# Kernel optimization log

Hardware: AMD Instinct MI355X
Metric: run time of the kernel (lower is better)

Reference implementation:

```python
import jax, jax.numpy as jnp
import numpy as np

NJ, NS = 30000, 12000            # num job / skill nodes
E_JS, E_SJ, E_SS = 300000, 300000, 150000
SBERT, HID, OUT = 384, 128, 128
H = 2                             # GAT heads (concat=True)
NEG_SLOPE = 0.2


def setup_inputs() -> dict:
    key = jax.random.key(0)
    ks = iter(jax.random.split(key, 64))
    nrm = lambda shape, s=1.0: jax.random.normal(next(ks), shape, jnp.float32) * s
    ridx = lambda n, hi: jax.random.randint(next(ks), (n,), 0, hi, jnp.int32)
    W = 0.05  # weight scale to keep activations sane across layers
    return dict(
        x_job=nrm((NJ, SBERT)), x_skill=nrm((NS, SBERT)),
        ei_js_src=ridx(E_JS, NJ), ei_js_dst=ridx(E_JS, NS),
        ei_sj_src=ridx(E_SJ, NS), ei_sj_dst=ridx(E_SJ, NJ),
        ei_ss_src=ridx(E_SS, NS), ei_ss_dst=ridx(E_SS, NS),
        query=nrm((SBERT,)),
        W0_job=nrm((SBERT, HID), W), b0_job=jnp.zeros((HID,), jnp.float32),
        g0_job=jnp.ones((HID,), jnp.float32), be0_job=jnp.zeros((HID,), jnp.float32),
        W0_skill=nrm((SBERT, HID), W), b0_skill=jnp.zeros((HID,), jnp.float32),
        g0_skill=jnp.ones((HID,), jnp.float32), be0_skill=jnp.zeros((HID,), jnp.float32),
        gat_Ws=nrm((2, 3, HID, H * HID), W), gat_Wd=nrm((2, 3, HID, H * HID), W),
        gat_as=nrm((2, 3, H, HID), W), gat_ad=nrm((2, 3, H, HID), W),
        gat_b=jnp.zeros((2, 3, H * HID), jnp.float32),
        inter_W=nrm((2, 2, H * HID, HID), W), inter_b=jnp.zeros((2, 2, HID), jnp.float32),
        Wjf=nrm((HID, OUT), W), bjf=jnp.zeros((OUT,), jnp.float32),
        Wq=nrm((SBERT, OUT), W), bq=jnp.zeros((OUT,), jnp.float32),
    )


def _layer_norm(x, g, b):
    mu = x.mean(-1, keepdims=True)
    var = ((x - mu) ** 2).mean(-1, keepdims=True)
    return (x - mu) * jax.lax.rsqrt(var + 1e-5) * g + b


def _gat(x_src, x_dst, src, dst, Ws, Wd, a_s, a_d, bias, num_dst):
    # PyG GATConv: lin_src/lin_dst (no bias), additive attention, scatter-softmax over dst.
    hs = (x_src @ Ws).reshape(-1, H, HID)            # [Ns,H,C]
    hd = (x_dst @ Wd).reshape(-1, H, HID)            # [Nd,H,C]
    e = jax.nn.leaky_relu((hs * a_s).sum(-1)[src] + (hd * a_d).sum(-1)[dst], NEG_SLOPE)  # [E,H]
    m = jax.ops.segment_max(e, dst, num_segments=num_dst)
    p = jnp.exp(e - m[dst])
    den = jax.ops.segment_sum(p, dst, num_segments=num_dst)
    w = p / (den[dst] + 1e-16)                       # [E,H]
    out = jax.ops.segment_sum(hs[src] * w[:, :, None], dst, num_segments=num_dst)
    return out.reshape(num_dst, H * HID) + bias


def _forward(x_job, x_skill, query,
             W0_job, b0_job, g0_job, be0_job, W0_skill, b0_skill, g0_skill, be0_skill,
             gat_Ws, gat_Wd, gat_as, gat_ad, gat_b, inter_W, inter_b, Wjf, bjf, Wq, bq,
             ei_js_src, ei_js_dst, ei_sj_src, ei_sj_dst, ei_ss_src, ei_ss_dst):
    # initial per-type lin + LN + relu (dropout = identity in eval)
    xj = jax.nn.relu(_layer_norm(x_job @ W0_job + b0_job, g0_job, be0_job))
    xs = jax.nn.relu(_layer_norm(x_skill @ W0_skill + b0_skill, g0_skill, be0_skill))
    # skill->skill relation adds self loops (src == dst node type)
    loops = jnp.arange(NS, dtype=jnp.int32)
    ss_src = jnp.concatenate([ei_ss_src, loops])
    ss_dst = jnp.concatenate([ei_ss_dst, loops])
    for i in range(2):  # num_layers
        o_s = (_gat(xj, xs, ei_js_src, ei_js_dst, gat_Ws[i, 0], gat_Wd[i, 0],
                    gat_as[i, 0], gat_ad[i, 0], gat_b[i, 0], NS)
               + _gat(xs, xs, ss_src, ss_dst, gat_Ws[i, 2], gat_Wd[i, 2],
                      gat_as[i, 2], gat_ad[i, 2], gat_b[i, 2], NS))  # HeteroConv aggr='sum'
        o_j = _gat(xs, xj, ei_sj_src, ei_sj_dst, gat_Ws[i, 1], gat_Wd[i, 1],
                   gat_as[i, 1], gat_ad[i, 1], gat_b[i, 1], NJ)
        xj = jax.nn.relu(o_j @ inter_W[i, 0] + inter_b[i, 0])
        xs = jax.nn.relu(o_s @ inter_W[i, 1] + inter_b[i, 1])
    job_emb = xj @ Wjf + bjf                          # [NJ,OUT]
    q = query @ Wq + bq                               # [OUT]
    scores = job_emb @ q                              # [NJ]
    return scores, job_emb, q


def reference(x_job, x_skill, ei_js_src, ei_js_dst, ei_sj_src, ei_sj_dst,
              ei_ss_src, ei_ss_dst, query,
              W0_job, b0_job, g0_job, be0_job, W0_skill, b0_skill, g0_skill, be0_skill,
              gat_Ws, gat_Wd, gat_as, gat_ad, gat_b, inter_W, inter_b,
              Wjf, bjf, Wq, bq):
    return _forward(x_job, x_skill, query,
                    W0_job, b0_job, g0_job, be0_job, W0_skill, b0_skill, g0_skill, be0_skill,
                    gat_Ws, gat_Wd, gat_as, gat_ad, gat_b, inter_W, inter_b, Wjf, bjf, Wq, bq,
                    ei_js_src, ei_js_dst, ei_sj_src, ei_sj_dst, ei_ss_src, ei_ss_dst)
```

## Files before the change

kernel.cpp:

```cpp
#include <hip/hip_runtime.h>
#include <hip/hip_bf16.h>
#include <math.h>

#define NJ 30000
#define NS 12000
#define E_JS 300000
#define E_SJ 300000
#define E_SS 150000
#define ETOT (E_JS + E_SJ + E_SS + NS)
#define NBINS (NS + NJ + NS)
#define NBUK ((NBINS + 63) / 64)
#define SBERT 384
#define HIST_NB 512
#define SCAT_NB 120
#define CAST_MATS 14
#define CAST_BPM 48
#define PREP_CAST (CAST_MATS * CAST_BPM)
#define PREP_WA   (PREP_CAST + 12)
#define PREP_QV   PREP_WA
#define PREP_GB   (PREP_QV + 1)
#define PREP_HIST (PREP_GB + 1)

static inline int cdiv(int a, int b) { return (a + b - 1) / b; }

typedef __attribute__((ext_vector_type(8))) short bf8_t;
typedef __attribute__((ext_vector_type(4))) float f4_t;
typedef unsigned short u16;

__device__ inline float bf2f(unsigned short u) {
    union { unsigned int i; float f; } z; z.i = ((unsigned int)u) << 16; return z.f;
}
__device__ inline unsigned short f2bf(float f) {
    unsigned int x = __float_as_uint(f);
    unsigned int r = (x + 0x7fffu + ((x >> 16) & 1u)) >> 16;
    return (unsigned short)r;
}

__device__ inline void edge_decode(int e, const int* js_src, const int* js_dst,
                                   const int* sj_src, const int* sj_dst,
                                   const int* ss_src, const int* ss_dst,
                                   int& src, int& bin) {
    if (e < E_JS) { src = js_src[e]; bin = js_dst[e]; }
    else if (e < E_JS + E_SJ) { int i = e - E_JS; src = sj_src[i]; bin = NS + sj_dst[i]; }
    else if (e < E_JS + E_SJ + E_SS) { int i = e - E_JS - E_SJ; src = ss_src[i]; bin = NS + NJ + ss_dst[i]; }
    else { int i = e - E_JS - E_SJ - E_SS; src = i; bin = NS + NJ + i; }
}

struct CastT { const float* src; unsigned short* dst; int K; int N; int srcLd; int dstLd; };
struct PrepArgs {
    CastT m[CAST_MATS];
    const float* Ws; const float* as_; const float* Wd; const float* ad_;
    float* wsa; float* wda; int* bcnt;
    const float* query; const float* Wq; const float* bq; float* qv;
    const float* gat_b; float* gbS;
    const int* js_src; const int* js_dst;
    const int* sj_src; const int* sj_dst;
    const int* ss_src; const int* ss_dst;
};

__global__ __launch_bounds__(256) void k_prep(PrepArgs A) {
    __shared__ float ldt[32][33];
    __shared__ int lh[NBUK];
    int b = blockIdx.x;
    if (b < PREP_CAST) {
        int mi = b / CAST_BPM, bx = b % CAST_BPM;
        CastT cm = A.m[mi];
        int tilesN = cm.N >> 5;
        int total = (cm.K >> 5) * tilesN;
        if (bx >= total) return;
        int tk = bx / tilesN, tn = bx % tilesN;
        int k0 = tk * 32, n0 = tn * 32;
        int col = threadIdx.x & 31;
        int row0 = threadIdx.x >> 5;
#pragma unroll
        for (int r = 0; r < 4; ++r) {
            int kk = row0 + r * 8;
            ldt[kk][col] = cm.src[(size_t)(k0 + kk) * cm.srcLd + n0 + col];
        }
        __syncthreads();
#pragma unroll
        for (int r = 0; r < 4; ++r) {
            int nn = row0 + r * 8;
            cm.dst[(size_t)(n0 + nn) * cm.dstLd + k0 + col] = f2bf(ldt[col][nn]);
        }
    } else if (b < PREP_WA) {
        int id = (b - PREP_CAST) * 256 + threadIdx.x;
        if (id >= 2 * 1536) return;
        int which = id / 1536;
        int r = id % 1536;
        int lr = r / 256;
        int kh = r % 256;
        int k = kh / 2, h = kh % 2;
        const float* W = which ? A.Wd : A.Ws;
        const float* a = which ? A.ad_ : A.as_;
        const float* wrow = W + ((size_t)(lr * 128 + k)) * 256 + h * 128;
        const float* arow = a + (size_t)(lr * 2 + h) * 128;
        float acc = 0.f;
        for (int c2 = 0; c2 < 128; ++c2) acc += wrow[c2] * arow[c2];
        (which ? A.wda : A.wsa)[lr * 256 + k * 2 + h] = acc;
    } else if (b == PREP_QV) {
        int c = threadIdx.x;
        if (c < 128) {
            float acc = A.bq[c];
            for (int k = 0; k < SBERT; ++k) acc += A.query[k] * A.Wq[(size_t)k * 128 + c];
            A.qv[c] = acc;
        }
    } else if (b == PREP_GB) {
        int c = threadIdx.x;
        if (c < 256) A.gbS[c] = A.gat_b[c] + A.gat_b[512 + c];
    } else {
        int t = threadIdx.x;
        for (int i = t; i < NBUK; i += 256) lh[i] = 0;
        __syncthreads();
        int hb = b - PREP_HIST;
        for (int e = hb * 256 + t; e < ETOT; e += HIST_NB * 256) {
            int src, bin;
            edge_decode(e, A.js_src, A.js_dst, A.sj_src, A.sj_dst, A.ss_src, A.ss_dst, src, bin);
            atomicAdd(&lh[bin >> 6], 1);
        }
        __syncthreads();
        for (int i = t; i < NBUK; i += 256) {
            int v = lh[i];
            if (v) atomicAdd(&A.bcnt[i], v);
        }
    }
}

struct GJob {
    const void* X; const unsigned short* Wt;
    const float* bias; const float* gamma; const float* beta;
    void* Y; int M; int K; int N; int ldY; int srcf32;
    const float* qv; float* sc;
    int aMode = 0;
    const float* wav0 = nullptr; const float* wav1 = nullptr;
    const float* wav2 = nullptr; const float* wav3 = nullptr;
    float* aOut = nullptr; int aStride = 0;
};
struct GPair { GJob a; GJob b; int blocksA; };

template <int EPI>
__device__ void mgemm_body(const GPair& P, int bx) {
    int mb = bx;
    GJob g = (mb < P.blocksA) ? P.a : P.b;
    if (mb >= P.blocksA) mb -= P.blocksA;
    const int row0 = mb * 64;

    __shared__ __align__(16) unsigned short Al[2][64][40];
    __shared__ __align__(16) unsigned short Bl[2][128][40];
    const int t = threadIdx.x;
    const int wave = t >> 6, lane = t & 63;
    const int q = lane >> 4, c = lane & 15;
    const int K = g.K;
    const int rA = t >> 2, cc8 = (t & 3) * 8;
    const int grA = row0 + rA;
    const bool inM = grA < g.M;
    const float* Xf = (const float*)g.X;

    f4_t acc[8];
#pragma unroll
    for (int nt = 0; nt < 8; ++nt) acc[nt] = (f4_t){0.f, 0.f, 0.f, 0.f};

    float4 a0[2], a1[2];
    uint4 b0[2], b1[2];

    auto LOAD = [&](int s, int k0) {
        if (inM) {
            const float* p = &Xf[(size_t)grA * K + k0 + cc8];
            a0[s] = *(const float4*)p;
            a1[s] = *(const float4*)(p + 4);
        } else {
            a0[s] = make_float4(0.f, 0.f, 0.f, 0.f);
            a1[s] = a0[s];
        }
        b0[s] = *(const uint4*)&g.Wt[(size_t)rA * K + k0 + cc8];
        b1[s] = *(const uint4*)&g.Wt[(size_t)(64 + rA) * K + k0 + cc8];
    };
    auto STORE = [&](int s, int cur) {
        ushort4 lo = make_ushort4(f2bf(a0[s].x), f2bf(a0[s].y), f2bf(a0[s].z), f2bf(a0[s].w));
        ushort4 hi = make_ushort4(f2bf(a1[s].x), f2bf(a1[s].y), f2bf(a1[s].z), f2bf(a1[s].w));
        *(ushort4*)&Al[cur][rA][cc8] = lo;
        *(ushort4*)&Al[cur][rA][cc8 + 4] = hi;
        *(uint4*)&Bl[cur][rA][cc8] = b0[s];
        *(uint4*)&Bl[cur][64 + rA][cc8] = b1[s];
    };
    auto MF = [&](int cur) {
        bf8_t af = *(const bf8_t*)&Al[cur][wave * 16 + c][q * 8];
#pragma unroll
        for (int nt = 0; nt < 8; ++nt) {
            bf8_t bfr = *(const bf8_t*)&Bl[cur][nt * 16 + c][q * 8];
            acc[nt] = __builtin_amdgcn_mfma_f32_16x16x32_bf16(af, bfr, acc[nt], 0, 0, 0);
        }
    };

    LOAD(0, 0);
    LOAD(1, 32);
    int cur = 0;
    for (int k0 = 0; k0 < K; k0 += 64) {
        STORE(0, cur);
        __syncthreads();
        if (k0 + 64 < K) LOAD(0, k0 + 64);
        MF(cur);
        cur ^= 1;
        STORE(1, cur);
        __syncthreads();
        if (k0 + 96 < K) LOAD(1, k0 + 96);
        MF(cur);
        cur ^= 1;
    }

    float bcol[8], gcol[8], becol[8];
#pragma unroll
    for (int nt = 0; nt < 8; ++nt) {
        bcol[nt] = g.bias[nt * 16 + c];
        if constexpr (EPI == 3) {
            gcol[nt] = g.gamma[nt * 16 + c];
            becol[nt] = g.beta[nt * 16 + c];
        }
    }

#pragma unroll
    for (int r = 0; r < 4; ++r) {
        int grow = row0 + wave * 16 + q * 4 + r;
        float v[8];
#pragma unroll
        for (int nt = 0; nt < 8; ++nt) v[nt] = acc[nt][r] + bcol[nt];
        if constexpr (EPI == 3) {
            float s = 0.f, ss = 0.f;
#pragma unroll
            for (int nt = 0; nt < 8; ++nt) { s += v[nt]; ss += v[nt] * v[nt]; }
#pragma unroll
            for (int m = 8; m >= 1; m >>= 1) {
                s += __shfl_xor(s, m, 64);
                ss += __shfl_xor(ss, m, 64);
            }
            float mu = s * (1.f / 128.f);
            float var = ss * (1.f / 128.f) - mu * mu;
            float rs = rsqrtf(var + 1e-5f);
#pragma unroll
            for (int nt = 0; nt < 8; ++nt)
                v[nt] = fmaxf((v[nt] - mu) * rs * gcol[nt] + becol[nt], 0.f);
        }
        if (g.aMode > 0) {
            float pa[8];
#pragma unroll
            for (int i = 0; i < 8; ++i) pa[i] = 0.f;
#pragma unroll
            for (int nt = 0; nt < 8; ++nt) {
                int col = nt * 16 + c;
                float2 w0 = *(const float2*)&g.wav0[col * 2];
                pa[0] += v[nt] * w0.x; pa[1] += v[nt] * w0.y;
                if (g.aMode > 1) {
                    float2 w1 = *(const float2*)&g.wav1[col * 2];
                    pa[2] += v[nt] * w1.x; pa[3] += v[nt] * w1.y;
                }
                if (g.aMode > 2) {
                    float2 w2 = *(const float2*)&g.wav2[col * 2];
                    float2 w3 = *(const float2*)&g.wav3[col * 2];
                    pa[4] += v[nt] * w2.x; pa[5] += v[nt] * w2.y;
                    pa[6] += v[nt] * w3.x; pa[7] += v[nt] * w3.y;
                }
            }
#pragma unroll
            for (int m = 8; m >= 1; m >>= 1) {
                pa[0] += __shfl_xor(pa[0], m, 64); pa[1] += __shfl_xor(pa[1], m, 64);
                pa[2] += __shfl_xor(pa[2], m, 64); pa[3] += __shfl_xor(pa[3], m, 64);
                pa[4] += __shfl_xor(pa[4], m, 64); pa[5] += __shfl_xor(pa[5], m, 64);
                pa[6] += __shfl_xor(pa[6], m, 64); pa[7] += __shfl_xor(pa[7], m, 64);
            }
            if (c == 0 && grow < g.M) {
                float* ao = &g.aOut[(size_t)grow * g.aStride];
                ao[0] = pa[0]; ao[1] = pa[1];
                if (g.aMode > 1) { ao[2] = pa[2]; ao[3] = pa[3]; }
                if (g.aMode > 2) { ao[4] = pa[4]; ao[5] = pa[5]; ao[6] = pa[6]; ao[7] = pa[7]; }
            }
        }
        if (grow < g.M) {
            unsigned short* Y = (unsigned short*)g.Y;
#pragma unroll
            for (int nt = 0; nt < 8; ++nt)
                Y[(size_t)grow * g.ldY + nt * 16 + c] = f2bf(v[nt]);
        }
    }
}

__global__ __launch_bounds__(256) void k_scan(
    const int* __restrict__ bcnt, int* __restrict__ bukoff, int* __restrict__ bukcur) {
    __shared__ int sd[256];
    int t = threadIdx.x;
    int i0 = t * 4;
    int v0 = (i0 < NBUK) ? bcnt[i0] : 0;
    int v1 = (i0 + 1 < NBUK) ? bcnt[i0 + 1] : 0;
    int v2 = (i0 + 2 < NBUK) ? bcnt[i0 + 2] : 0;
    int v3 = (i0 + 3 < NBUK) ? bcnt[i0 + 3] : 0;
    int csum = v0 + v1 + v2 + v3;
    sd[t] = csum;
    __syncthreads();
    for (int off = 1; off < 256; off <<= 1) {
        int tmp = (t >= off) ? sd[t - off] : 0;
        __syncthreads();
        sd[t] += tmp;
        __syncthreads();
    }
    int excl = sd[t] - csum;
    int p0 = excl, p1 = excl + v0, p2 = excl + v0 + v1, p3 = excl + v0 + v1 + v2;
    if (i0 < NBUK) { bukoff[i0] = p0; bukcur[i0] = p0; }
    if (i0 + 1 < NBUK) { bukoff[i0 + 1] = p1; bukcur[i0 + 1] = p1; }
    if (i0 + 2 < NBUK) { bukoff[i0 + 2] = p2; bukcur[i0 + 2] = p2; }
    if (i0 + 3 < NBUK) { bukoff[i0 + 3] = p3; bukcur[i0 + 3] = p3; }
    if (t == 0) bukoff[NBUK] = ETOT;
}

__global__ __launch_bounds__(256) void k_lin0_scat(
    GPair P, int gemmBlocks,
    const int* __restrict__ js_src, const int* __restrict__ js_dst,
    const int* __restrict__ sj_src, const int* __restrict__ sj_dst,
    const int* __restrict__ ss_src, const int* __restrict__ ss_dst,
    int* __restrict__ bukcur, uint2* __restrict__ pairs) {
    if (blockIdx.x < (unsigned)gemmBlocks) {
        mgemm_body<3>(P, blockIdx.x);
        return;
    }
    __shared__ int lh[NBUK];
    __shared__ int lbase[NBUK];
    int t = threadIdx.x;
    int sb = blockIdx.x - gemmBlocks;
    const int CH = (ETOT + SCAT_NB - 1) / SCAT_NB;
    const int beg = sb * CH;
    const int endi = (beg + CH < ETOT) ? beg + CH : ETOT;
    for (int i = t; i < NBUK; i += 256) lh[i] = 0;
    __syncthreads();
    for (int e = beg + t; e < endi; e += 256) {
        int src, bin;
        edge_decode(e, js_src, js_dst, sj_src, sj_dst, ss_src, ss_dst, src, bin);
        atomicAdd(&lh[bin >> 6], 1);
    }
    __syncthreads();
    for (int i = t; i < NBUK; i += 256) {
        int v = lh[i];
        lbase[i] = v ? atomicAdd(&bukcur[i], v) : 0;
    }
    __syncthreads();
    for (int i = t; i < NBUK; i += 256) lh[i] = 0;
    __syncthreads();
    for (int e = beg + t; e < endi; e += 256) {
        int src, bin;
        edge_decode(e, js_src, js_dst, sj_src, sj_dst, ss_src, ss_dst, src, bin);
        int bu = bin >> 6;
        int pos = lbase[bu] + atomicAdd(&lh[bu], 1);
        pairs[pos] = make_uint2((unsigned)src, (unsigned)bin);
    }
}

__global__ __launch_bounds__(256) void k_finalize(
    const uint2* __restrict__ pairs, const int* __restrict__ bukoff,
    int* __restrict__ offs, int* __restrict__ esrc) {
    int b = blockIdx.x, t = threadIdx.x;
    int base = bukoff[b], endi = bukoff[b + 1];
    __shared__ int cnt[64], excl[64], curs[64];
    if (t < 64) cnt[t] = 0;
    __syncthreads();
    for (int i = base + t; i < endi; i += 256)
        atomicAdd(&cnt[pairs[i].y & 63], 1);
    __syncthreads();
    if (t < 64) {
        int v = cnt[t];
        int inc = v;
#pragma unroll
        for (int off = 1; off < 64; off <<= 1) {
            int tmp = __shfl_up(inc, off, 64);
            if (t >= off) inc += tmp;
        }
        excl[t] = inc - v;
        curs[t] = inc - v;
    }
    __syncthreads();
    for (int i = base + t; i < endi; i += 256) {
        uint2 p = pairs[i];
        int lb = p.y & 63;
        int pos = atomicAdd(&curs[lb], 1);
        esrc[base + pos] = (int)p.x;
    }
    if (t < 64) {
        int bin = b * 64 + t;
        if (bin < NBINS) offs[bin] = base + excl[t];
    }
    if (b == 0 && t == 0) offs[NBINS] = ETOT;
}

__device__ inline void fm8(float p0, float p1, uint4 u, float a0[8], float a1[8]) {
    float x0 = __uint_as_float(u.x << 16);
    float x1 = __uint_as_float(u.x & 0xffff0000u);
    float x2 = __uint_as_float(u.y << 16);
    float x3 = __uint_as_float(u.y & 0xffff0000u);
    float x4 = __uint_as_float(u.z << 16);
    float x5 = __uint_as_float(u.z & 0xffff0000u);
    float x6 = __uint_as_float(u.w << 16);
    float x7 = __uint_as_float(u.w & 0xffff0000u);
    a0[0] += p0 * x0; a0[1] += p0 * x1; a0[2] += p0 * x2; a0[3] += p0 * x3;
    a0[4] += p0 * x4; a0[5] += p0 * x5; a0[6] += p0 * x6; a0[7] += p0 * x7;
    a1[0] += p1 * x0; a1[1] += p1 * x1; a1[2] += p1 * x2; a1[3] += p1 * x3;
    a1[4] += p1 * x4; a1[5] += p1 * x5; a1[6] += p1 * x6; a1[7] += p1 * x7;
}

__device__ inline void rel_run(
    const int* __restrict__ esrc, int beg, int end,
    const float* __restrict__ aSrc, int aShift, int aOff, float adx, float ady,
    const unsigned short* __restrict__ rows, int colOff, int g,
    float a0[8], float a1[8], float& den0, float& den1) {
    int j = beg;
    for (; j + 8 <= end; j += 8) {
        int s0 = esrc[j + g];
        int s1 = esrc[j + 4 + g];
        uint4 u0 = *(const uint4*)&rows[(unsigned)s0 * 128 + colOff];
        uint4 u1 = *(const uint4*)&rows[(unsigned)s1 * 128 + colOff];
        float2 f0 = *(const float2*)&aSrc[((unsigned)s0 << aShift) + aOff];
        float2 f1 = *(const float2*)&aSrc[((unsigned)s1 << aShift) + aOff];
        float e00 = f0.x + adx; e00 = e00 > 0.f ? e00 : 0.2f * e00;
        float e01 = f0.y + ady; e01 = e01 > 0.f ? e01 : 0.2f * e01;
        float e10 = f1.x + adx; e10 = e10 > 0.f ? e10 : 0.2f * e10;
        float e11 = f1.y + ady; e11 = e11 > 0.f ? e11 : 0.2f * e11;
        float p00 = __expf(e00), p01 = __expf(e01);
        float p10 = __expf(e10), p11 = __expf(e11);
        fm8(p00, p01, u0, a0, a1);
        fm8(p10, p11, u1, a0, a1);
        den0 += p00 + p10; den1 += p01 + p11;
    }
    for (; j < end; j += 4) {
        int e = j + g;
        bool ok = e < end;
        int s = esrc[ok ? e : j];
        uint4 u = *(const uint4*)&rows[(unsigned)s * 128 + colOff];
        float2 f = *(const float2*)&aSrc[((unsigned)s << aShift) + aOff];
        float e0 = f.x + adx; e0 = e0 > 0.f ? e0 : 0.2f * e0;
        float e1 = f.y + ady; e1 = e1 > 0.f ? e1 : 0.2f * e1;
        float p0 = ok ? __expf(e0) : 0.f;
        float p1 = ok ? __expf(e1) : 0.f;
        fm8(p0, p1, u, a0, a1);
        den0 += p0; den1 += p1;
    }
}

__device__ inline void store8(unsigned short* dst, const float v[8]) {
    uint4 o;
    o.x = (unsigned)f2bf(v[0]) | ((unsigned)f2bf(v[1]) << 16);
    o.y = (unsigned)f2bf(v[2]) | ((unsigned)f2bf(v[3]) << 16);
    o.z = (unsigned)f2bf(v[4]) | ((unsigned)f2bf(v[5]) << 16);
    o.w = (unsigned)f2bf(v[6]) | ((unsigned)f2bf(v[7]) << 16);
    *(uint4*)dst = o;
}

__device__ inline void finish_store(float a0[8], float a1[8], float den0, float den1,
                                    int lane, unsigned short* base) {
    float d0 = den0; d0 += __shfl_xor(d0, 16, 64); d0 += __shfl_xor(d0, 32, 64);
    float d1 = den1; d1 += __shfl_xor(d1, 16, 64); d1 += __shfl_xor(d1, 32, 64);
    float s0 = 1.f / (d0 + 1e-16f), s1 = 1.f / (d1 + 1e-16f);
    float o0[8], o1[8];
#pragma unroll
    for (int i = 0; i < 8; ++i) {
        float t0 = a0[i]; t0 += __shfl_xor(t0, 16, 64); t0 += __shfl_xor(t0, 32, 64);
        float t1 = a1[i]; t1 += __shfl_xor(t1, 16, 64); t1 += __shfl_xor(t1, 32, 64);
        o0[i] = t0 * s0; o1[i] = t1 * s1;
    }
    if ((lane >> 4) == 0) {
        store8(base, o0);
        store8(base + 128, o1);
    }
}

__global__ __launch_bounds__(256) void k_gather_all(
    const int* __restrict__ offs, const int* __restrict__ esrc,
    const float* __restrict__ aJ, const float* __restrict__ aS,
    const unsigned short* __restrict__ rowsJ,
    const unsigned short* __restrict__ rowsS,
    unsigned short* __restrict__ aggS,
    unsigned short* __restrict__ aggJ,
    int jobOnly) {
    int wave = threadIdx.x >> 6, lane = threadIdx.x & 63;
    int idx = blockIdx.x * 4 + wave;
    int g = lane >> 4, cl = lane & 15;
    int colOff = cl * 8;

    float a0[8], a1[8], den0, den1;

    if (jobOnly) {
        if (idx >= NJ) return;
        int d = idx;
#pragma unroll
        for (int i = 0; i < 8; ++i) { a0[i] = 0.f; a1[i] = 0.f; }
        den0 = den1 = 0.f;
        int bb = NS + d;
        float2 ad = *(const float2*)&aJ[(unsigned)d * 4 + 2];
        rel_run(esrc, offs[bb], offs[bb + 1], aS, 3, 4, ad.x, ad.y, rowsS, colOff, g, a0, a1, den0, den1);
        finish_store(a0, a1, den0, den1, lane, &aggJ[(size_t)d * 256 + colOff]);
        return;
    }
    if (idx < NS) {
        int d = idx;
#pragma unroll
        for (int i = 0; i < 8; ++i) { a0[i] = 0.f; a1[i] = 0.f; }
        den0 = den1 = 0.f;
        float2 adA = *(const float2*)&aS[(unsigned)d * 8 + 2];
        rel_run(esrc, offs[d], offs[d + 1], aJ, 2, 0, adA.x, adA.y, rowsJ, colOff, g, a0, a1, den0, den1);
        finish_store(a0, a1, den0, den1, lane, &aggS[(size_t)d * 512 + colOff]);
#pragma unroll
        for (int i = 0; i < 8; ++i) { a0[i] = 0.f; a1[i] = 0.f; }
        den0 = den1 = 0.f;
        int bb = NS + NJ + d;
        float2 adB = *(const float2*)&aS[(unsigned)d * 8 + 6];
        rel_run(esrc, offs[bb], offs[bb + 1], aS, 3, 0, adB.x, adB.y, rowsS, colOff, g, a0, a1, den0, den1);
        finish_store(a0, a1, den0, den1, lane, &aggS[(size_t)d * 512 + 256 + colOff]);
    } else if (idx < NS + NJ) {
        int d = idx - NS;
#pragma unroll
        for (int i = 0; i < 8; ++i) { a0[i] = 0.f; a1[i] = 0.f; }
        den0 = den1 = 0.f;
        int bb = NS + d;
        float2 ad = *(const float2*)&aJ[(unsigned)d * 4 + 2];
        rel_run(esrc, offs[bb], offs[bb + 1], aS, 3, 4, ad.x, ad.y, rowsS, colOff, g, a0, a1, den0, den1);
        finish_store(a0, a1, den0, den1, lane, &aggJ[(size_t)d * 256 + colOff]);
    }
}

struct FJob {
    const unsigned short* X; int K1; int M;
    const unsigned short* Wt1; const float* bias1;
    const unsigned short* Wt2; const float* bias2;
    const float* wa; float* aOut; int aStride;
    unsigned short* Y2;
};
struct FPair { FJob a; FJob b; int blocksA; };

__global__ __launch_bounds__(256) void k_fused2(FPair P) {
    int mb = blockIdx.x;
    FJob g = (mb < P.blocksA) ? P.a : P.b;
    if (mb >= P.blocksA) mb -= P.blocksA;
    const int row0 = mb * 64;
    const int K1 = g.K1;

    __shared__ __align__(16) unsigned short Al[64][40];
    __shared__ __align__(16) unsigned short Bl[128][40];
    __shared__ __align__(16) unsigned short Y1l[4][64][40];
    const int t = threadIdx.x;
    const int wave = t >> 6, lane = t & 63;
    const int q = lane >> 4, c = lane & 15;

    f4_t acc2[8];
#pragma unroll
    for (int nt = 0; nt < 8; ++nt) acc2[nt] = (f4_t){0.f, 0.f, 0.f, 0.f};

    for (int np = 0; np < 2; ++np) {
        f4_t acc[8];
#pragma unroll
        for (int nt = 0; nt < 8; ++nt) acc[nt] = (f4_t){0.f, 0.f, 0.f, 0.f};
        for (int k0 = 0; k0 < K1; k0 += 32) {
#pragma unroll
            for (int it = 0; it < 3; ++it) {
                int idx = t + it * 256;
                int r = idx >> 2, cc = (idx & 3) * 8;
                if (r < 64) {
                    int gr = row0 + r;
                    uint4 va = (gr < g.M) ? *(const uint4*)&g.X[(size_t)gr * K1 + k0 + cc]
                                          : make_uint4(0u, 0u, 0u, 0u);
                    *(uint4*)&Al[r][cc] = va;
                } else {
                    int br = r - 64;
                    *(uint4*)&Bl[br][cc] = *(const uint4*)&g.Wt1[(size_t)(np * 128 + br) * K1 + k0 + cc];
                }
            }
            __syncthreads();
            bf8_t af = *(const bf8_t*)&Al[wave * 16 + c][q * 8];
#pragma unroll
            for (int nt = 0; nt < 8; ++nt) {
                bf8_t bfr = *(const bf8_t*)&Bl[nt * 16 + c][q * 8];
                acc[nt] = __builtin_amdgcn_mfma_f32_16x16x32_bf16(af, bfr, acc[nt], 0, 0, 0);
            }
            __syncthreads();
        }
        float bcol[8];
#pragma unroll
        for (int nt = 0; nt < 8; ++nt) bcol[nt] = g.bias1[np * 128 + nt * 16 + c];
#pragma unroll
        for (int r = 0; r < 4; ++r) {
            int row = wave * 16 + q * 4 + r;
#pragma unroll
            for (int nt = 0; nt < 8; ++nt)
                Y1l[nt >> 1][row][(nt & 1) * 16 + c] = f2bf(acc[nt][r] + bcol[nt]);
        }
        __syncthreads();
        for (int k0 = 0; k0 < 128; k0 += 32) {
#pragma unroll
            for (int it = 0; it < 2; ++it) {
                int idx = t + it * 256;
                int br = idx >> 2, cc = (idx & 3) * 8;
                *(uint4*)&Bl[br][cc] = *(const uint4*)&g.Wt2[(size_t)br * 256 + np * 128 + k0 + cc];
            }
            __syncthreads();
            bf8_t af = *(const bf8_t*)&Y1l[k0 >> 5][wave * 16 + c][q * 8];
#pragma unroll
            for (int nt = 0; nt < 8; ++nt) {
                bf8_t bfr = *(const bf8_t*)&Bl[nt * 16 + c][q * 8];
                acc2[nt] = __builtin_amdgcn_mfma_f32_16x16x32_bf16(af, bfr, acc2[nt], 0, 0, 0);
            }
            __syncthreads();
        }
    }

    float b2[8];
#pragma unroll
    for (int nt = 0; nt < 8; ++nt) b2[nt] = g.bias2[nt * 16 + c];
#pragma unroll
    for (int r = 0; r < 4; ++r) {
        int grow = row0 + wave * 16 + q * 4 + r;
        float v[8];
#pragma unroll
        for (int nt = 0; nt < 8; ++nt) v[nt] = fmaxf(acc2[nt][r] + b2[nt], 0.f);
        if (g.wa) {
            float pa0 = 0.f, pa1 = 0.f;
#pragma unroll
            for (int nt = 0; nt < 8; ++nt) {
                float2 w0 = *(const float2*)&g.wa[(nt * 16 + c) * 2];
                pa0 += v[nt] * w0.x; pa1 += v[nt] * w0.y;
            }
#pragma unroll
            for (int m = 8; m >= 1; m >>= 1) {
                pa0 += __shfl_xor(pa0, m, 64);
                pa1 += __shfl_xor(pa1, m, 64);
            }
            if (c == 0 && grow < g.M) {
                g.aOut[(size_t)grow * g.aStride + 0] = pa0;
                g.aOut[(size_t)grow * g.aStride + 1] = pa1;
            }
        }
        if (g.Y2 && grow < g.M) {
#pragma unroll
            for (int nt = 0; nt < 8; ++nt)
                g.Y2[(size_t)grow * 128 + nt * 16 + c] = f2bf(v[nt]);
        }
    }
}

struct F3 {
    const unsigned short* X; int M;
    const unsigned short* Wt1; const float* bias1;
    const unsigned short* Wt2; const float* bias2;
    const unsigned short* Wt3; const float* bias3;
    const float* qv; float* sc; float* Y;
};

__global__ __launch_bounds__(256) void k_fused3(F3 g) {
    int mb = blockIdx.x;
    const int row0 = mb * 64;
    __shared__ __align__(16) unsigned short Al[64][40];
    __shared__ __align__(16) unsigned short Bl[128][40];
    __shared__ __align__(16) unsigned short Yl[4][64][40];
    const int t = threadIdx.x;
    const int wave = t >> 6, lane = t & 63;
    const int q = lane >> 4, c = lane & 15;

    f4_t acc2[8];
#pragma unroll
    for (int nt = 0; nt < 8; ++nt) acc2[nt] = (f4_t){0.f, 0.f, 0.f, 0.f};

    for (int np = 0; np < 2; ++np) {
        f4_t acc[8];
#pragma unroll
        for (int nt = 0; nt < 8; ++nt) acc[nt] = (f4_t){0.f, 0.f, 0.f, 0.f};
        for (int k0 = 0; k0 < 256; k0 += 32) {
#pragma unroll
            for (int it = 0; it < 3; ++it) {
                int idx = t + it * 256;
                int r = idx >> 2, cc = (idx & 3) * 8;
                if (r < 64) {
                    int gr = row0 + r;
                    uint4 va = (gr < g.M) ? *(const uint4*)&g.X[(size_t)gr * 256 + k0 + cc]
                                          : make_uint4(0u, 0u, 0u, 0u);
                    *(uint4*)&Al[r][cc] = va;
                } else {
                    int br = r - 64;
                    *(uint4*)&Bl[br][cc] = *(const uint4*)&g.Wt1[(size_t)(np * 128 + br) * 256 + k0 + cc];
                }
            }
            __syncthreads();
            bf8_t af = *(const bf8_t*)&Al[wave * 16 + c][q * 8];
#pragma unroll
            for (int nt = 0; nt < 8; ++nt) {
                bf8_t bfr = *(const bf8_t*)&Bl[nt * 16 + c][q * 8];
                acc[nt] = __builtin_amdgcn_mfma_f32_16x16x32_bf16(af, bfr, acc[nt], 0, 0, 0);
            }
            __syncthreads();
        }
        float bcol[8];
#pragma unroll
        for (int nt = 0; nt < 8; ++nt) bcol[nt] = g.bias1[np * 128 + nt * 16 + c];
#pragma unroll
        for (int r = 0; r < 4; ++r) {
            int row = wave * 16 + q * 4 + r;
#pragma unroll
            for (int nt = 0; nt < 8; ++nt)
                Yl[nt >> 1][row][(nt & 1) * 16 + c] = f2bf(acc[nt][r] + bcol[nt]);
        }
        __syncthreads();
        for (int k0 = 0; k0 < 128; k0 += 32) {
#pragma unroll
            for (int it = 0; it < 2; ++it) {
                int idx = t + it * 256;
                int br = idx >> 2, cc = (idx & 3) * 8;
                *(uint4*)&Bl[br][cc] = *(const uint4*)&g.Wt2[(size_t)br * 256 + np * 128 + k0 + cc];
            }
            __syncthreads();
            bf8_t af = *(const bf8_t*)&Yl[k0 >> 5][wave * 16 + c][q * 8];
#pragma unroll
            for (int nt = 0; nt < 8; ++nt) {
                bf8_t bfr = *(const bf8_t*)&Bl[nt * 16 + c][q * 8];
                acc2[nt] = __builtin_amdgcn_mfma_f32_16x16x32_bf16(af, bfr, acc2[nt], 0, 0, 0);
            }
            __syncthreads();
        }
    }

    {
        float b2[8];
#pragma unroll
        for (int nt = 0; nt < 8; ++nt) b2[nt] = g.bias2[nt * 16 + c];
#pragma unroll
        for (int r = 0; r < 4; ++r) {
            int row = wave * 16 + q * 4 + r;
#pragma unroll
            for (int nt = 0; nt < 8; ++nt)
                Yl[nt >> 1][row][(nt & 1) * 16 + c] = f2bf(fmaxf(acc2[nt][r] + b2[nt], 0.f));
        }
        __syncthreads();
    }

    f4_t acc3[8];
#pragma unroll
    for (int nt = 0; nt < 8; ++nt) acc3[nt] = (f4_t){0.f, 0.f, 0.f, 0.f};
    for (int k0 = 0; k0 < 128; k0 += 32) {
#pragma unroll
        for (int it = 0; it < 2; ++it) {
            int idx = t + it * 256;
            int br = idx >> 2, cc = (idx & 3) * 8;
            *(uint4*)&Bl[br][cc] = *(const uint4*)&g.Wt3[(size_t)br * 128 + k0 + cc];
        }
        __syncthreads();
        bf8_t af = *(const bf8_t*)&Yl[k0 >> 5][wave * 16 + c][q * 8];
#pragma unroll
        for (int nt = 0; nt < 8; ++nt) {
            bf8_t bfr = *(const bf8_t*)&Bl[nt * 16 + c][q * 8];
            acc3[nt] = __builtin_amdgcn_mfma_f32_16x16x32_bf16(af, bfr, acc3[nt], 0, 0, 0);
        }
        __syncthreads();
    }
    float b3[8], qcol[8];
#pragma unroll
    for (int nt = 0; nt < 8; ++nt) {
        b3[nt] = g.bias3[nt * 16 + c];
        qcol[nt] = g.qv[nt * 16 + c];
    }
#pragma unroll
    for (int r = 0; r < 4; ++r) {
        int grow = row0 + wave * 16 + q * 4 + r;
        float v[8];
#pragma unroll
        for (int nt = 0; nt < 8; ++nt) v[nt] = acc3[nt][r] + b3[nt];
        float part = 0.f;
#pragma unroll
        for (int nt = 0; nt < 8; ++nt) part += v[nt] * qcol[nt];
#pragma unroll
        for (int m = 8; m >= 1; m >>= 1) part += __shfl_xor(part, m, 64);
        if (grow < g.M) {
            if (c == 0) g.sc[grow] = part;
#pragma unroll
            for (int nt = 0; nt < 8; ++nt)
                g.Y[(size_t)grow * 128 + nt * 16 + c] = v[nt];
        }
    }
}

extern "C" void kernel_launch(void* const* d_in, const int* in_sizes, int n_in,
                              void* d_out, int out_size, void* d_ws, size_t ws_size,
                              hipStream_t stream) {
    const float* x_job   = (const float*)d_in[0];
    const float* x_skill = (const float*)d_in[1];
    const int* js_src = (const int*)d_in[2];
    const int* js_dst = (const int*)d_in[3];
    const int* sj_src = (const int*)d_in[4];
    const int* sj_dst = (const int*)d_in[5];
    const int* ss_src = (const int*)d_in[6];
    const int* ss_dst = (const int*)d_in[7];
    const float* query    = (const float*)d_in[8];
    const float* W0_job   = (const float*)d_in[9];
    const float* b0_job   = (const float*)d_in[10];
    const float* g0_job   = (const float*)d_in[11];
    const float* be0_job  = (const float*)d_in[12];
    const float* W0_skill = (const float*)d_in[13];
    const float* b0_skill = (const float*)d_in[14];
    const float* g0_skill = (const float*)d_in[15];
    const float* be0_skill= (const float*)d_in[16];
    const float* gat_Ws = (const float*)d_in[17];
    const float* gat_Wd = (const float*)d_in[18];
    const float* gat_as = (const float*)d_in[19];
    const float* gat_ad = (const float*)d_in[20];
    const float* gat_b  = (const float*)d_in[21];
    const float* inter_W = (const float*)d_in[22];
    const float* inter_b = (const float*)d_in[23];
    const float* Wjf = (const float*)d_in[24];
    const float* bjf = (const float*)d_in[25];
    const float* Wq  = (const float*)d_in[26];
    const float* bq  = (const float*)d_in[27];

    char* w = (char*)d_ws;
    auto alloc = [&](size_t bytes) -> void* {
        void* p = (void*)w;
        w += (bytes + 255) & ~(size_t)255;
        return p;
    };
    u16* xj   = (u16*)alloc((size_t)NJ * 128 * 2);
    u16* xs   = (u16*)alloc((size_t)NS * 128 * 2);
    u16* xs1  = (u16*)alloc((size_t)NS * 128 * 2);
    u16* aggJ  = (u16*)alloc((size_t)NJ * 256 * 2);
    u16* aggJ1 = (u16*)alloc((size_t)NJ * 256 * 2);
    u16* aggS  = (u16*)alloc((size_t)NS * 512 * 2);
    u16* WtW0j = (u16*)alloc((size_t)SBERT * 128 * 2);
    u16* WtW0s = (u16*)alloc((size_t)SBERT * 128 * 2);
    u16* WsS1  = (u16*)alloc((size_t)256 * 512 * 2);
    u16* WsJ0  = (u16*)alloc((size_t)256 * 256 * 2);
    u16* WsJ1  = (u16*)alloc((size_t)256 * 256 * 2);
    u16* WtI00 = (u16*)alloc((size_t)128 * 256 * 2);
    u16* WtI01 = (u16*)alloc((size_t)128 * 256 * 2);
    u16* WtI10 = (u16*)alloc((size_t)128 * 256 * 2);
    u16* WtJf  = (u16*)alloc((size_t)128 * 128 * 2);
    float* gbS = (float*)alloc(256 * 4);
    float* aJ = (float*)alloc((size_t)NJ * 4 * 4);
    float* aS = (float*)alloc((size_t)NS * 8 * 4);
    float* wsa = (float*)alloc(6 * 256 * 4);
    float* wda = (float*)alloc(6 * 256 * 4);
    int* bcnt   = (int*)alloc((size_t)NBUK * 4);
    int* bukoff = (int*)alloc((size_t)(NBUK + 1) * 4);
    int* bukcur = (int*)alloc((size_t)NBUK * 4);
    uint2* pairs = (uint2*)alloc((size_t)ETOT * 8);
    int* offs = (int*)alloc((size_t)(NBINS + 1) * 4);
    int* esrc = (int*)alloc((size_t)ETOT * 4);

    float* out = (float*)d_out;
    float* scores  = out;
    float* job_emb = out + NJ;
    float* qv      = out + NJ + (size_t)NJ * 128;

    const int mbJ = cdiv(NJ, 64);
    const int mbS = cdiv(NS, 64);
    const int gemmB = mbJ + mbS;

    hipMemsetAsync(bcnt, 0, (size_t)NBUK * 4, stream);
    hipMemsetAsync(WsS1, 0, (size_t)256 * 512 * 2, stream);
    hipMemsetAsync(WsJ0, 0, (size_t)256 * 256 * 2, stream);
    hipMemsetAsync(WsJ1, 0, (size_t)256 * 256 * 2, stream);

    {
        const size_t WS = (size_t)128 * 256;
        const size_t IW = (size_t)256 * 128;
        PrepArgs A;
        A.m[0]  = {W0_job,   WtW0j, SBERT, 128, 128, SBERT};
        A.m[1]  = {W0_skill, WtW0s, SBERT, 128, 128, SBERT};
        A.m[2]  = {gat_Ws + 0 * WS,       WsS1,                       128, 128, 256, 512};
        A.m[3]  = {gat_Ws + 0 * WS + 128, WsS1 + 128 * 512 + 128,     128, 128, 256, 512};
        A.m[4]  = {gat_Ws + 2 * WS,       WsS1 + 256,                 128, 128, 256, 512};
        A.m[5]  = {gat_Ws + 2 * WS + 128, WsS1 + 128 * 512 + 384,     128, 128, 256, 512};
        A.m[6]  = {gat_Ws + 1 * WS,       WsJ0,                       128, 128, 256, 256};
        A.m[7]  = {gat_Ws + 1 * WS + 128, WsJ0 + 128 * 256 + 128,     128, 128, 256, 256};
        A.m[8]  = {gat_Ws + 4 * WS,       WsJ1,                       128, 128, 256, 256};
        A.m[9]  = {gat_Ws + 4 * WS + 128, WsJ1 + 128 * 256 + 128,     128, 128, 256, 256};
        A.m[10] = {inter_W + 0 * IW, WtI00, 256, 128, 128, 256};
        A.m[11] = {inter_W + 1 * IW, WtI01, 256, 128, 128, 256};
        A.m[12] = {inter_W + 2 * IW, WtI10, 256, 128, 128, 256};
        A.m[13] = {Wjf, WtJf, 128, 128, 128, 128};
        A.Ws = gat_Ws; A.as_ = gat_as; A.Wd = gat_Wd; A.ad_ = gat_ad;
        A.wsa = wsa; A.wda = wda; A.bcnt = bcnt;
        A.query = query; A.Wq = Wq; A.bq = bq; A.qv = qv;
        A.gat_b = gat_b; A.gbS = gbS;
        A.js_src = js_src; A.js_dst = js_dst;
        A.sj_src = sj_src; A.sj_dst = sj_dst;
        A.ss_src = ss_src; A.ss_dst = ss_dst;
        k_prep<<<PREP_HIST + HIST_NB, 256, 0, stream>>>(A);
    }

    k_scan<<<1, 256, 0, stream>>>(bcnt, bukoff, bukcur);

    {
        GPair P;
        P.a = {x_job, WtW0j, b0_job, g0_job, be0_job, xj, NJ, SBERT, 128, 128, 1,
               nullptr, nullptr, 2, wsa + 0, wda + 256, nullptr, nullptr, aJ, 4};
        P.b = {x_skill, WtW0s, b0_skill, g0_skill, be0_skill, xs, NS, SBERT, 128, 128, 1,
               nullptr, nullptr, 4, wsa + 2 * 256, wda + 0, wsa + 1 * 256, wda + 2 * 256, aS, 8};
        P.blocksA = mbJ;
        k_lin0_scat<<<gemmB + SCAT_NB, 256, 0, stream>>>(
            P, gemmB, js_src, js_dst, sj_src, sj_dst, ss_src, ss_dst, bukcur, pairs);
    }

    k_finalize<<<NBUK, 256, 0, stream>>>(pairs, bukoff, offs, esrc);

    k_gather_all<<<cdiv(NS + NJ, 4), 256, 0, stream>>>(
        offs, esrc, aJ, aS, xj, xs, aggS, aggJ, 0);

    {
        FPair P;
        P.a = {aggJ, 256, NJ, WsJ0, gat_b + 256, WtI00, inter_b + 0,
               wda + 4 * 256, aJ + 2, 4, nullptr};
        P.b = {aggS, 512, NS, WsS1, gbS, WtI01, inter_b + 128,
               wsa + 4 * 256, aS + 4, 8, xs1};
        P.blocksA = mbJ;
        k_fused2<<<gemmB, 256, 0, stream>>>(P);
    }

    k_gather_all<<<cdiv(NJ, 4), 256, 0, stream>>>(
        offs, esrc, aJ, aS, nullptr, xs1, nullptr, aggJ1, 1);

    {
        F3 g3;
        g3.X = aggJ1; g3.M = NJ;
        g3.Wt1 = WsJ1; g3.bias1 = gat_b + 4 * 256;
        g3.Wt2 = WtI10; g3.bias2 = inter_b + 2 * 128;
        g3.Wt3 = WtJf; g3.bias3 = bjf;
        g3.qv = qv; g3.sc = scores; g3.Y = job_emb;
        k_fused3<<<mbJ, 256, 0, stream>>>(g3);
    }
}
```

Before: 353.1 us.

## Stage GEMM tiles via direct global-to-LDS loads with swizzle; widen edge scatter grid

The GEMM mainloop now copies fp32 activation and bf16 weight tiles straight from global memory into XOR-swizzled LDS buffers using global_load_lds, instead of staging them through registers. The fp32-to-bf16 conversion moves to fragment-read time, and the K step shrinks to 32 with a single double buffer. The aim is to cut register pressure and the store-to-LDS instructions, and to overlap loads with MFMA. The cost is double the LDS footprint for the A tile and conversion work repeated by each wave. Separately, the edge scatter uses four times as many blocks, with an early exit for blocks that have no edges.

Result: faster. 330.4 us (-6.4%).

```diff
diff --git a/kernel.cpp b/kernel.cpp
--- a/kernel.cpp
+++ b/kernel.cpp
@@ -12,7 +12,7 @@
 #define NBUK ((NBINS + 63) / 64)
 #define SBERT 384
 #define HIST_NB 512
-#define SCAT_NB 120
+#define SCAT_NB 480
 #define CAST_MATS 14
 #define CAST_BPM 48
 #define PREP_CAST (CAST_MATS * CAST_BPM)
@@ -145,65 +145,68 @@
     if (mb >= P.blocksA) mb -= P.blocksA;
     const int row0 = mb * 64;
 
-    __shared__ __align__(16) unsigned short Al[2][64][40];
-    __shared__ __align__(16) unsigned short Bl[2][128][40];
+    __shared__ __align__(16) float As[2][64][32];
+    __shared__ __align__(16) unsigned short Bs[2][128][32];
     const int t = threadIdx.x;
     const int wave = t >> 6, lane = t & 63;
     const int q = lane >> 4, c = lane & 15;
     const int K = g.K;
-    const int rA = t >> 2, cc8 = (t & 3) * 8;
-    const int grA = row0 + rA;
-    const bool inM = grA < g.M;
     const float* Xf = (const float*)g.X;
 
     f4_t acc[8];
 #pragma unroll
     for (int nt = 0; nt < 8; ++nt) acc[nt] = (f4_t){0.f, 0.f, 0.f, 0.f};
 
-    float4 a0[2], a1[2];
-    uint4 b0[2], b1[2];
-
-    auto LOAD = [&](int s, int k0) {
-        if (inM) {
-            const float* p = &Xf[(size_t)grA * K + k0 + cc8];
-            a0[s] = *(const float4*)p;
-            a1[s] = *(const float4*)(p + 4);
-        } else {
-            a0[s] = make_float4(0.f, 0.f, 0.f, 0.f);
-            a1[s] = a0[s];
-        }
-        b0[s] = *(const uint4*)&g.Wt[(size_t)rA * K + k0 + cc8];
-        b1[s] = *(const uint4*)&g.Wt[(size_t)(64 + rA) * K + k0 + cc8];
+    auto STAGE = [&](int cur, int k0) {
+#pragma unroll
+        for (int i = 0; i < 2; ++i) {
+            int bi = i * 256 + t;
+            int row = bi >> 3, b = bi & 7;
+            int ra = row0 + row; ra = (ra < g.M) ? ra : (g.M - 1);
+            const float* gsrc = Xf + (size_t)ra * K + k0 + ((b ^ (row & 7)) << 2);
+            __builtin_amdgcn_global_load_lds(
+                (__attribute__((address_space(1))) void*)gsrc,
+                (__attribute__((address_space(3))) void*)((char*)&As[cur][0][0] + ((i * 4 + wave) << 10)),
+                16, 0, 0);
+        }
+#pragma unroll
+        for (int i = 0; i < 2; ++i) {
+            int bi = i * 256 + t;
+            int row = bi >> 2, b = bi & 3;
+            const unsigned short* gsrc = g.Wt + (size_t)row * K + k0 + ((b ^ ((row >> 1) & 3)) << 3);
+            __builtin_amdgcn_global_load_lds(
+                (__attribute__((address_space(1))) void*)gsrc,
+                (__attribute__((address_space(3))) void*)((char*)&Bs[cur][0][0] + ((i * 4 + wave) << 10)),
+                16, 0, 0);
+        }
     };
-    auto STORE = [&](int s, int cur) {
-        ushort4 lo = make_ushort4(f2bf(a0[s].x), f2bf(a0[s].y), f2bf(a0[s].z), f2bf(a0[s].w));
-        ushort4 hi = make_ushort4(f2bf(a1[s].x), f2bf(a1[s].y), f2bf(a1[s].z), f2bf(a1[s].w));
-        *(ushort4*)&Al[cur][rA][cc8] = lo;
-        *(ushort4*)&Al[cur][rA][cc8 + 4] = hi;
-        *(uint4*)&Bl[cur][rA][cc8] = b0[s];
-        *(uint4*)&Bl[cur][64 + rA][cc8] = b1[s];
+
+    auto MF = [&](int cur) {
+        const char* Ab = (const char*)&As[cur][0][0];
+        const char* Bb = (const char*)&Bs[cur][0][0];
+        int r = wave * 16 + c;
+        int sw = r & 7;
+        f4_t fa0 = *(const f4_t*)(Ab + r * 128 + (((q * 2) ^ sw) << 4));
+        f4_t fa1 = *(const f4_t*)(Ab + r * 128 + (((q * 2 + 1) ^ sw) << 4));
+        bf8_t af;
+        af[0] = (short)f2bf(fa0[0]); af[1] = (short)f2bf(fa0[1]);
+        af[2] = (short)f2bf(fa0[2]); af[3] = (short)f2bf(fa0[3]);
+        af[4] = (short)f2bf(fa1[0]); af[5] = (short)f2bf(fa1[1]);
+        af[6] = (short)f2bf(fa1[2]); af[7] = (short)f2bf(fa1[3]);
+#pragma unroll
+        for (int nt = 0; nt < 8; ++nt) {
+            int rb = nt * 16 + c;
+            bf8_t bfr = *(const bf8_t*)(Bb + rb * 64 + ((q ^ ((rb >> 1) & 3)) << 4));
+            acc[nt] = __builtin_amdgcn_mfma_f32_16x16x32_bf16(af, bfr, acc[nt], 0, 0, 0);
+        }
     };
-    auto MF = [&](int cur) {
-        bf8_t af = *(const bf8_t*)&Al[cur][wave * 16 + c][q * 8];
-#pragma unroll
-        for (int nt = 0; nt < 8; ++nt) {
-            bf8_t bfr = *(const bf8_t*)&Bl[cur][nt * 16 + c][q * 8];
-            acc[nt] = __builtin_amdgcn_mfma_f32_16x16x32_bf16(af, bfr, acc[nt], 0, 0, 0);
-        }
-    };
-
-    LOAD(0, 0);
-    LOAD(1, 32);
+
+    STAGE(0, 0);
     int cur = 0;
-    for (int k0 = 0; k0 < K; k0 += 64) {
-        STORE(0, cur);
-        __syncthreads();
-        if (k0 + 64 < K) LOAD(0, k0 + 64);
-        MF(cur);
-        cur ^= 1;
-        STORE(1, cur);
-        __syncthreads();
-        if (k0 + 96 < K) LOAD(1, k0 + 96);
+    for (int k0 = 0; k0 < K; k0 += 32) {
+        asm volatile("s_waitcnt vmcnt(0)" ::: "memory");
+        __syncthreads();
+        if (k0 + 32 < K) STAGE(cur ^ 1, k0 + 32);
         MF(cur);
         cur ^= 1;
     }
@@ -327,6 +330,7 @@
     const int CH = (ETOT + SCAT_NB - 1) / SCAT_NB;
     const int beg = sb * CH;
     const int endi = (beg + CH < ETOT) ? beg + CH : ETOT;
+    if (beg >= ETOT) return;
     for (int i = t; i < NBUK; i += 256) lh[i] = 0;
     __syncthreads();
     for (int e = beg + t; e < endi; e += 256) {
```
